# Optimization experiments

Hardware: AMD Instinct MI355X
Metric: run time of the kernel (lower is better)

## Reference

```python
import jax, jax.numpy as jnp
import numpy as np

E = 8          # num_experts
D = 768        # d_model
H = 3072       # d_hidden
TOP_K = 2


def setup_inputs() -> dict:
    key = jax.random.key(0)
    ks = jax.random.split(key, 8)
    s_in = 1.0 / np.sqrt(D)
    s_h = 1.0 / np.sqrt(H)
    return {
        "hidden_states": jax.random.normal(ks[0], (2, 2048, D), dtype=jnp.float32),
        "gate_w": jax.random.normal(ks[1], (E, D), dtype=jnp.float32) * s_in,
        "gate_b": jnp.zeros((E,), dtype=jnp.float32),
        "w1": jax.random.normal(ks[2], (E, H, D), dtype=jnp.float32) * s_in,  # FMoELinear: [E, out, in]
        "b1": jnp.zeros((E, H), dtype=jnp.float32),
        "w2": jax.random.normal(ks[3], (E, D, H), dtype=jnp.float32) * s_h,
        "b2": jnp.zeros((E, D), dtype=jnp.float32),
        "bias": jnp.zeros((D,), dtype=jnp.float32),
    }


def reference(hidden_states, gate_w, gate_b, w1, b1, w2, b2, bias):
    B, S, d = hidden_states.shape
    x = hidden_states.reshape(-1, d)                      # [T, D]
    T = x.shape[0]
    # NaiveGate: linear gate, top-k, softmax over the top-k logits
    logits = x @ gate_w.T + gate_b                        # [T, E]
    top_val, top_idx = jax.lax.top_k(logits, TOP_K)       # [T, K]
    scores = jax.nn.softmax(top_val, axis=-1)             # [T, K]
    # combine weights: [T, E], score mass scattered to chosen experts
    combine = jnp.zeros((T, E), dtype=x.dtype)
    combine = combine.at[jnp.arange(T)[:, None], top_idx].add(scores)
    # expert MLPs (dense over experts, masked combine keeps routing math exact)
    h = jnp.einsum('td,ehd->teh', x, w1) + b1             # [T, E, H]
    h = jax.nn.gelu(h, approximate=False)                 # torch F.gelu (exact erf)
    y = jnp.einsum('teh,edh->ted', h, w2) + b2            # [T, E, D]
    out = jnp.einsum('te,ted->td', combine, y)            # [T, D]
    return out.reshape(B, S, d), bias
```

## Files before the change

kernel.cpp:

```cpp
#include <hip/hip_runtime.h>
#include <hip/hip_bf16.h>

#define DD 768
#define HH 3072
#define NE 8
#define TOPK 2

#define BK 64
#define CAP 1536
#define NRBMAX (CAP/128)
#define NB1 (HH / 128)
#define NB2 (DD / 128)

typedef __attribute__((ext_vector_type(8))) short short8;
typedef __attribute__((ext_vector_type(4))) float f32x4;

static __device__ __forceinline__ unsigned short f2bf(float v) {
    __hip_bfloat16 b = __float2bfloat16(v);
    return *reinterpret_cast<unsigned short*>(&b);
}

static __device__ __forceinline__ float gelu_f(float v) {
    float s = v * 0.70710678118f;
    float a = fabsf(s);
    float t = __builtin_amdgcn_rcpf(1.f + 0.3275911f * a);
    float poly = t * (0.254829592f + t * (-0.284496736f + t * (1.421413741f +
                 t * (-1.453152027f + t * 1.061405429f))));
    float erfv = 1.f - poly * __expf(-s * s);
    erfv = copysignf(erfv, s);
    return 0.5f * v * (1.f + erfv);
}

__global__ __launch_bounds__(256) void convert_kernel(
    const float* __restrict__ w1, const float* __restrict__ w2,
    unsigned short* __restrict__ w1b, unsigned short* __restrict__ w2b,
    int* __restrict__ ctrl, int* __restrict__ qcur, size_t n)
{
    size_t tid = (size_t)blockIdx.x * blockDim.x + threadIdx.x;
    if (tid < 64) ctrl[tid] = 0;
    if (tid < 256) qcur[tid] = 0;
    size_t stride = (size_t)gridDim.x * blockDim.x;
    size_t quarter = n / 4;
    size_t tot = 2 * quarter;
    for (size_t j = tid; j < tot; j += stride) {
        const float* src; unsigned short* dst; size_t off;
        if (j < quarter) { src = w1; dst = w1b; off = j * 4; }
        else             { src = w2; dst = w2b; off = (j - quarter) * 4; }
        float4 v = *reinterpret_cast<const float4*>(&src[off]);
        ushort4 o;
        o.x = f2bf(v.x); o.y = f2bf(v.y); o.z = f2bf(v.z); o.w = f2bf(v.w);
        *reinterpret_cast<ushort4*>(&dst[off]) = o;
    }
}

__global__ __launch_bounds__(256) void route_kernel(
    const float* __restrict__ x, const float* __restrict__ gw, const float* __restrict__ gb,
    int* __restrict__ ctrl, int* __restrict__ pos_of, float* __restrict__ wpos,
    unsigned short* __restrict__ Xe, int T, int maxP)
{
    __shared__ int s_e[32], s_rank[32];
    __shared__ float s_w[32];
    __shared__ int lh[NE], lbase[NE];

    int tid = threadIdx.x;
    if (tid < NE) lh[tid] = 0;
    __syncthreads();

    int w = tid >> 6, lane = tid & 63;

#pragma unroll
    for (int j = 0; j < 4; ++j) {
        int t = blockIdx.x * 16 + w * 4 + j;
        if (t >= T) break;
        float acc[NE];
#pragma unroll
        for (int e = 0; e < NE; ++e) acc[e] = 0.f;
        const float4* xr = reinterpret_cast<const float4*>(x + (size_t)t * DD);
#pragma unroll
        for (int k = 0; k < 3; ++k) {
            float4 xv = xr[k * 64 + lane];
#pragma unroll
            for (int e = 0; e < NE; ++e) {
                float4 gv = *reinterpret_cast<const float4*>(&gw[e * DD + (k * 64 + lane) * 4]);
                acc[e] += xv.x * gv.x + xv.y * gv.y + xv.z * gv.z + xv.w * gv.w;
            }
        }
#pragma unroll
        for (int e = 0; e < NE; ++e) {
            float v = acc[e];
            for (int off = 32; off; off >>= 1) v += __shfl_xor(v, off, 64);
            acc[e] = v;
        }
        if (lane == 0) {
            float lg[NE];
#pragma unroll
            for (int e = 0; e < NE; ++e) lg[e] = acc[e] + gb[e];
            int i0 = 0;
#pragma unroll
            for (int e = 1; e < NE; ++e) if (lg[e] > lg[i0]) i0 = e;
            int i1 = -1;
#pragma unroll
            for (int e = 0; e < NE; ++e) {
                if (e == i0) continue;
                if (i1 < 0 || lg[e] > lg[i1]) i1 = e;
            }
            float m = lg[i0];
            float e0 = __expf(lg[i0] - m), e1 = __expf(lg[i1] - m);
            float s = e0 + e1;
            int slot = (w * 4 + j) * 2;
            s_e[slot]     = i0; s_w[slot]     = e0 / s; s_rank[slot]     = atomicAdd(&lh[i0], 1);
            s_e[slot + 1] = i1; s_w[slot + 1] = e1 / s; s_rank[slot + 1] = atomicAdd(&lh[i1], 1);
        }
    }
    __syncthreads();

    if (tid < NE) lbase[tid] = lh[tid] ? atomicAdd(&ctrl[8 + tid], lh[tid]) : 0;
    __syncthreads();

#pragma unroll
    for (int j = 0; j < 4; ++j) {
        int t = blockIdx.x * 16 + w * 4 + j;
        if (t >= T) break;
        const float4* xr = reinterpret_cast<const float4*>(x + (size_t)t * DD);
        ushort4 o[3];
#pragma unroll
        for (int k = 0; k < 3; ++k) {
            float4 v = xr[k * 64 + lane];
            o[k].x = f2bf(v.x); o[k].y = f2bf(v.y); o[k].z = f2bf(v.z); o[k].w = f2bf(v.w);
        }
#pragma unroll
        for (int s = 0; s < 2; ++s) {
            int slot = (w * 4 + j) * 2 + s;
            int e = s_e[slot];
            int p = e * CAP + lbase[e] + s_rank[slot];
            p = min(p, maxP - 1);
            if (lane == 0) { pos_of[2 * t + s] = p; wpos[p] = s_w[slot]; }
#pragma unroll
            for (int k = 0; k < 3; ++k)
                *reinterpret_cast<ushort4*>(&Xe[(size_t)p * DD + (k * 64 + lane) * 4]) = o[k];
        }
    }
}

__global__ void offsets_kernel(int* ctrl, int* wq1, int* wq2)
{
    if (threadIdx.x == 0 && blockIdx.x == 0) {
        int nrbs[NE];
        for (int e = 0; e < NE; ++e) {
            int cnt = ctrl[8 + e];
            int nrb = (cnt + 127) >> 7;
            nrbs[e] = nrb > NRBMAX ? NRBMAX : nrb;
        }
        int qc[8], qcum[8];
        for (int q = 0; q < 8; ++q) { qc[q] = 0; qcum[q] = 0; }
        for (int pair = 0; pair < NE * NB1; ++pair) {
            int e = pair / NB1;
            int q = pair & 7;
            int s = qc[q]++;
            qcum[q] += nrbs[e];
            wq1[(q * 24 + s) * 2 + 0] = pair;
            wq1[(q * 24 + s) * 2 + 1] = qcum[q];
        }
        for (int q = 0; q < 8; ++q) { qc[q] = 0; qcum[q] = 0; }
        for (int g = 0; g < NE * NB2; ++g) {
            int e = g / NB2;
            int q = g & 7;
            int s = qc[q]++;
            qcum[q] += nrbs[e];
            wq2[(q * 6 + s) * 2 + 0] = g;
            wq2[(q * 6 + s) * 2 + 1] = qcum[q];
        }
    }
}

static __device__ __forceinline__ void stage_tile(
    const unsigned short* __restrict__ g, int ld, unsigned short* __restrict__ lds)
{
    int tid = threadIdx.x;
#pragma unroll
    for (int r = 0; r < 4; ++r) {
        int j = (r << 8) + tid;
        int row = j >> 3;
        int kc = (j & 7) ^ (row & 7);
        __builtin_amdgcn_global_load_lds(
            (const __attribute__((address_space(1))) void*)(g + (size_t)row * ld + (kc << 3)),
            (__attribute__((address_space(3))) void*)(lds + (j << 3)),
            16, 0, 0);
    }
}

#define LDSF(base, row, kc) \
    reinterpret_cast<const short8*>(&(base)[((((row) << 3) + ((kc) ^ ((row) & 7))) << 3)])

static __device__ __forceinline__ void gemm_item(
    const unsigned short* __restrict__ Abase,
    const unsigned short* __restrict__ Bbase,
    int ld, int nt,
    unsigned short* __restrict__ As, unsigned short* __restrict__ Bs,
    f32x4 acc[4][4], int wr, int wc, int fr, int fq)
{
    const int BUF = 128 * 64;
    stage_tile(Abase, ld, As);
    stage_tile(Bbase, ld, Bs);
    for (int t = 0; t < nt; ++t) {
        int cur = t & 1;
        if (t + 1 < nt) {
            stage_tile(Abase + (size_t)(t + 1) * BK, ld, As + (cur ^ 1) * BUF);
            stage_tile(Bbase + (size_t)(t + 1) * BK, ld, Bs + (cur ^ 1) * BUF);
            asm volatile("s_waitcnt vmcnt(8)" ::: "memory");
        } else {
            asm volatile("s_waitcnt vmcnt(0)" ::: "memory");
        }
        __builtin_amdgcn_s_barrier();
        asm volatile("" ::: "memory");

        const unsigned short* A = As + cur * BUF;
        const unsigned short* B = Bs + cur * BUF;
        short8 a[2][4], b[2][4];
#pragma unroll
        for (int ks = 0; ks < 2; ++ks) {
            int kc = ks * 4 + fq;
#pragma unroll
            for (int m = 0; m < 4; ++m)
                a[ks][m] = *LDSF(A, wr + m * 16 + fr, kc);
#pragma unroll
            for (int n = 0; n < 4; ++n)
                b[ks][n] = *LDSF(B, wc + n * 16 + fr, kc);
        }
        __builtin_amdgcn_s_setprio(1);
#pragma unroll
        for (int ks = 0; ks < 2; ++ks)
#pragma unroll
            for (int m = 0; m < 4; ++m)
#pragma unroll
                for (int n = 0; n < 4; ++n)
                    acc[m][n] = __builtin_amdgcn_mfma_f32_16x16x32_bf16(
                        b[ks][n], a[ks][m], acc[m][n], 0, 0, 0);
        __builtin_amdgcn_s_setprio(0);
        asm volatile("s_waitcnt lgkmcnt(0)" ::: "memory");
        __builtin_amdgcn_s_barrier();
        asm volatile("" ::: "memory");
    }
}


__global__ __launch_bounds__(256, 2) void gemm1_kernel(
    const unsigned short* __restrict__ Xe, const unsigned short* __restrict__ W1b,
    const float* __restrict__ b1, unsigned short* __restrict__ H1,
    const int* __restrict__ wq1, int* __restrict__ qcur)
{
    __shared__ unsigned short As[2 * 128 * 64];
    __shared__ unsigned short Bs[2 * 128 * 64];
    __shared__ int sh_item;
    __shared__ int tpair[192], tcum[192];

    int tid = threadIdx.x;
    if (tid < 192) { tpair[tid] = wq1[2 * tid]; tcum[tid] = wq1[2 * tid + 1]; }
    __syncthreads();

    int lane = tid & 63, w = tid >> 6;
    int wr = (w >> 1) * 64, wc = (w & 1) * 64;
    int fr = lane & 15, fq = lane >> 4;
    int q0 = blockIdx.x & 7;

    for (int off = 0; off < 8; ++off) {
        int qq = (q0 + off) & 7;
        int qtot = tcum[qq * 24 + 23];
        for (;;) {
            if (tid == 0) sh_item = atomicAdd(&qcur[qq * 16], 1);
            __syncthreads();
            int j = sh_item;
            __syncthreads();
            if (j >= qtot) break;

            int s = 0;
            while (tcum[qq * 24 + s] <= j) ++s;
            int pair = tpair[qq * 24 + s];
            int start = s ? tcum[qq * 24 + s - 1] : 0;
            int rb = j - start;
            int e = pair / NB1, cb = pair - e * NB1;
            int rowbase = e * CAP + (rb << 7);
            int colbase = cb << 7;

            const unsigned short* Abase = Xe + (size_t)rowbase * DD;
            const unsigned short* Bbase = W1b + (size_t)e * HH * DD + (size_t)colbase * DD;

            f32x4 acc[4][4];
#pragma unroll
            for (int m = 0; m < 4; ++m)
#pragma unroll
                for (int n = 0; n < 4; ++n) acc[m][n] = (f32x4){0.f, 0.f, 0.f, 0.f};

            gemm_item(Abase, Bbase, DD, DD / BK, As, Bs, acc, wr, wc, fr, fq);

            float4 bb[4];
#pragma unroll
            for (int n = 0; n < 4; ++n)
                bb[n] = *reinterpret_cast<const float4*>(
                    &b1[e * HH + colbase + wc + n * 16 + fq * 4]);
#pragma unroll
            for (int m = 0; m < 4; ++m) {
                int tok = rowbase + wr + m * 16 + fr;
#pragma unroll
                for (int n = 0; n < 4; ++n) {
                    int ch = colbase + wc + n * 16 + fq * 4;
                    ushort4 o;
                    o.x = f2bf(gelu_f(acc[m][n][0] + bb[n].x));
                    o.y = f2bf(gelu_f(acc[m][n][1] + bb[n].y));
                    o.z = f2bf(gelu_f(acc[m][n][2] + bb[n].z));
                    o.w = f2bf(gelu_f(acc[m][n][3] + bb[n].w));
                    *reinterpret_cast<ushort4*>(&H1[(size_t)tok * HH + ch]) = o;
                }
            }
        }
    }
}

__global__ __launch_bounds__(256, 2) void gemm2_kernel(
    const unsigned short* __restrict__ H1, const unsigned short* __restrict__ W2b,
    const float* __restrict__ b2, const float* __restrict__ wpos,
    float* __restrict__ Yb, const int* __restrict__ wq2, int* __restrict__ qcur)
{
    __shared__ unsigned short As[2 * 128 * 64];
    __shared__ unsigned short Bs[2 * 128 * 64];
    __shared__ int sh_item;
    __shared__ int tpair[48], tcum[48];

    int tid = threadIdx.x;
    if (tid < 48) { tpair[tid] = wq2[2 * tid]; tcum[tid] = wq2[2 * tid + 1]; }
    __syncthreads();

    int lane = tid & 63, w = tid >> 6;
    int wr = (w >> 1) * 64, wc = (w & 1) * 64;
    int fr = lane & 15, fq = lane >> 4;
    int q0 = blockIdx.x & 7;

    for (int off = 0; off < 8; ++off) {
        int qq = (q0 + off) & 7;
        int qtot = tcum[qq * 6 + 5];
        for (;;) {
            if (tid == 0) sh_item = atomicAdd(&qcur[(8 + qq) * 16], 1);
            __syncthreads();
            int j = sh_item;
            __syncthreads();
            if (j >= qtot) break;

            int s = 0;
            while (tcum[qq * 6 + s] <= j) ++s;
            int g = tpair[qq * 6 + s];
            int start = s ? tcum[qq * 6 + s - 1] : 0;
            int rb = j - start;
            int e = g / NB2, cb = g - e * NB2;
            int rowbase = e * CAP + (rb << 7);
            int colbase = cb << 7;

            const unsigned short* Abase = H1 + (size_t)rowbase * HH;
            const unsigned short* Bbase = W2b + (size_t)e * DD * HH + (size_t)colbase * HH;

            f32x4 acc[4][4];
#pragma unroll
            for (int m = 0; m < 4; ++m)
#pragma unroll
                for (int n = 0; n < 4; ++n) acc[m][n] = (f32x4){0.f, 0.f, 0.f, 0.f};

            gemm_item(Abase, Bbase, HH, HH / BK, As, Bs, acc, wr, wc, fr, fq);

            float4 bb[4];
#pragma unroll
            for (int n = 0; n < 4; ++n)
                bb[n] = *reinterpret_cast<const float4*>(
                    &b2[e * DD + colbase + wc + n * 16 + fq * 4]);
#pragma unroll
            for (int m = 0; m < 4; ++m) {
                int tok = rowbase + wr + m * 16 + fr;
                float wp = wpos[tok];
#pragma unroll
                for (int n = 0; n < 4; ++n) {
                    int ch = colbase + wc + n * 16 + fq * 4;
                    float4 o;
                    o.x = wp * (acc[m][n][0] + bb[n].x);
                    o.y = wp * (acc[m][n][1] + bb[n].y);
                    o.z = wp * (acc[m][n][2] + bb[n].z);
                    o.w = wp * (acc[m][n][3] + bb[n].w);
                    *reinterpret_cast<float4*>(&Yb[(size_t)tok * DD + ch]) = o;
                }
            }
        }
    }
}

__global__ __launch_bounds__(256) void combine_kernel(
    const float* __restrict__ Yb, const int* __restrict__ pos_of,
    const float* __restrict__ bias, float* __restrict__ out, int T)
{
    int i = blockIdx.x * blockDim.x + threadIdx.x;
    int total = T * (DD / 4);
    if (i < total) {
        int t = i / (DD / 4);
        int c = (i % (DD / 4)) * 4;
        int p0 = pos_of[2 * t], p1 = pos_of[2 * t + 1];
        float4 v0 = *reinterpret_cast<const float4*>(&Yb[(size_t)p0 * DD + c]);
        float4 v1 = *reinterpret_cast<const float4*>(&Yb[(size_t)p1 * DD + c]);
        float4 o;
        o.x = v0.x + v1.x; o.y = v0.y + v1.y;
        o.z = v0.z + v1.z; o.w = v0.w + v1.w;
        *reinterpret_cast<float4*>(&out[(size_t)t * DD + c]) = o;
    } else if (i < total + DD / 4) {
        int c = (i - total) * 4;
        *reinterpret_cast<float4*>(&out[(size_t)T * DD + c]) =
            *reinterpret_cast<const float4*>(&bias[c]);
    }
}

extern "C" void kernel_launch(void* const* d_in, const int* in_sizes, int n_in,
                              void* d_out, int out_size, void* d_ws, size_t ws_size,
                              hipStream_t stream)
{
    const float* x    = (const float*)d_in[0];
    const float* gw   = (const float*)d_in[1];
    const float* gb   = (const float*)d_in[2];
    const float* w1   = (const float*)d_in[3];
    const float* b1   = (const float*)d_in[4];
    const float* w2   = (const float*)d_in[5];
    const float* b2   = (const float*)d_in[6];
    const float* bias = (const float*)d_in[7];
    float* out = (float*)d_out;

    int T = in_sizes[0] / DD;
    int nA = T * TOPK;
    int maxP = NE * CAP + 256;

    char* ws = (char*)d_ws;
    size_t off = 0;
    auto alloc = [&](size_t bytes) -> char* {
        char* p = ws + off;
        off += (bytes + 255) & ~(size_t)255;
        return p;
    };
    unsigned short* w1b = (unsigned short*)alloc((size_t)NE * HH * DD * 2);
    unsigned short* w2b = (unsigned short*)alloc((size_t)NE * DD * HH * 2);
    unsigned short* Xe  = (unsigned short*)alloc((size_t)maxP * DD * 2);
    unsigned short* H1  = (unsigned short*)alloc((size_t)maxP * HH * 2);
    float*  Yb          = (float*)alloc((size_t)maxP * DD * 4);
    int*    pos_of      = (int*)alloc((size_t)nA * 4);
    float*  wpos        = (float*)alloc((size_t)maxP * 4);
    int*    ctrl        = (int*)alloc(64 * 4);
    int*    wq1         = (int*)alloc(384 * 4);
    int*    wq2         = (int*)alloc(96 * 4);
    int*    qcur        = (int*)alloc(256 * 4);

    size_t nW = (size_t)NE * HH * DD;

    hipLaunchKernelGGL(convert_kernel, dim3(4096), dim3(256), 0, stream,
                       w1, w2, w1b, w2b, ctrl, qcur, nW);
    hipLaunchKernelGGL(route_kernel, dim3((T + 15) / 16), dim3(256), 0, stream,
                       x, gw, gb, ctrl, pos_of, wpos, Xe, T, maxP);
    hipLaunchKernelGGL(offsets_kernel, dim3(1), dim3(64), 0, stream, ctrl, wq1, wq2);
    hipLaunchKernelGGL(gemm1_kernel, dim3(512), dim3(256), 0, stream,
                       Xe, w1b, b1, H1, wq1, qcur);
    hipLaunchKernelGGL(gemm2_kernel, dim3(512), dim3(256), 0, stream,
                       H1, w2b, b2, wpos, Yb, wq2, qcur);
    hipLaunchKernelGGL(combine_kernel, dim3((T * (DD / 4) + DD / 4 + 255) / 256, 1, 1), dim3(256), 0, stream,
                       Yb, pos_of, bias, out, T);
}
```

Before: 240.2 us.

## Fuse weight conversion into routing and gemm1 tails to overlap with compute

Removes the standalone fp32-to-bf16 conversion kernel. The w1 conversion now runs inside the routing kernel on a grid of at least 2048 blocks, and the w2 conversion runs as work-stealing tail chunks at the end of gemm1, claimed through an atomic counter. Control counters are zeroed with memsets instead. The aim is to hide conversion bandwidth behind routing and the gemm1 tail and to save a launch, at the cost of extra gemm1 work and possible contention with its memory traffic.

```diff
diff --git a/kernel.cpp b/kernel.cpp
--- a/kernel.cpp
+++ b/kernel.cpp
@@ -31,115 +31,108 @@
     return 0.5f * v * (1.f + erfv);
 }
 
-__global__ __launch_bounds__(256) void convert_kernel(
-    const float* __restrict__ w1, const float* __restrict__ w2,
-    unsigned short* __restrict__ w1b, unsigned short* __restrict__ w2b,
-    int* __restrict__ ctrl, int* __restrict__ qcur, size_t n)
-{
-    size_t tid = (size_t)blockIdx.x * blockDim.x + threadIdx.x;
-    if (tid < 64) ctrl[tid] = 0;
-    if (tid < 256) qcur[tid] = 0;
-    size_t stride = (size_t)gridDim.x * blockDim.x;
-    size_t quarter = n / 4;
-    size_t tot = 2 * quarter;
-    for (size_t j = tid; j < tot; j += stride) {
-        const float* src; unsigned short* dst; size_t off;
-        if (j < quarter) { src = w1; dst = w1b; off = j * 4; }
-        else             { src = w2; dst = w2b; off = (j - quarter) * 4; }
-        float4 v = *reinterpret_cast<const float4*>(&src[off]);
-        ushort4 o;
-        o.x = f2bf(v.x); o.y = f2bf(v.y); o.z = f2bf(v.z); o.w = f2bf(v.w);
-        *reinterpret_cast<ushort4*>(&dst[off]) = o;
-    }
-}
-
-__global__ __launch_bounds__(256) void route_kernel(
+static __device__ __forceinline__ void cvt4(const float* __restrict__ src,
+                                            unsigned short* __restrict__ dst, size_t j4)
+{
+    float4 v = *reinterpret_cast<const float4*>(&src[j4 * 4]);
+    ushort4 o;
+    o.x = f2bf(v.x); o.y = f2bf(v.y); o.z = f2bf(v.z); o.w = f2bf(v.w);
+    *reinterpret_cast<ushort4*>(&dst[j4 * 4]) = o;
+}
+
+__global__ __launch_bounds__(256) void routecvt_kernel(
     const float* __restrict__ x, const float* __restrict__ gw, const float* __restrict__ gb,
     int* __restrict__ ctrl, int* __restrict__ pos_of, float* __restrict__ wpos,
-    unsigned short* __restrict__ Xe, int T, int maxP)
+    unsigned short* __restrict__ Xe, int T, int maxP,
+    const float* __restrict__ w1, unsigned short* __restrict__ w1b, size_t n1_4)
 {
     __shared__ int s_e[32], s_rank[32];
     __shared__ float s_w[32];
     __shared__ int lh[NE], lbase[NE];
 
     int tid = threadIdx.x;
-    if (tid < NE) lh[tid] = 0;
-    __syncthreads();
-
     int w = tid >> 6, lane = tid & 63;
 
-#pragma unroll
-    for (int j = 0; j < 4; ++j) {
-        int t = blockIdx.x * 16 + w * 4 + j;
-        if (t >= T) break;
-        float acc[NE];
-#pragma unroll
-        for (int e = 0; e < NE; ++e) acc[e] = 0.f;
-        const float4* xr = reinterpret_cast<const float4*>(x + (size_t)t * DD);
-#pragma unroll
-        for (int k = 0; k < 3; ++k) {
-            float4 xv = xr[k * 64 + lane];
+    if ((int)blockIdx.x * 16 < T) {
+        if (tid < NE) lh[tid] = 0;
+        __syncthreads();
+
+#pragma unroll
+        for (int j = 0; j < 4; ++j) {
+            int t = blockIdx.x * 16 + w * 4 + j;
+            if (t >= T) break;
+            float acc[NE];
+#pragma unroll
+            for (int e = 0; e < NE; ++e) acc[e] = 0.f;
+            const float4* xr = reinterpret_cast<const float4*>(x + (size_t)t * DD);
+#pragma unroll
+            for (int k = 0; k < 3; ++k) {
+                float4 xv = xr[k * 64 + lane];
+#pragma unroll
+                for (int e = 0; e < NE; ++e) {
+                    float4 gv = *reinterpret_cast<const float4*>(&gw[e * DD + (k * 64 + lane) * 4]);
+                    acc[e] += xv.x * gv.x + xv.y * gv.y + xv.z * gv.z + xv.w * gv.w;
+                }
+            }
 #pragma unroll
             for (int e = 0; e < NE; ++e) {
-                float4 gv = *reinterpret_cast<const float4*>(&gw[e * DD + (k * 64 + lane) * 4]);
-                acc[e] += xv.x * gv.x + xv.y * gv.y + xv.z * gv.z + xv.w * gv.w;
-            }
-        }
-#pragma unroll
-        for (int e = 0; e < NE; ++e) {
-            float v = acc[e];
-            for (int off = 32; off; off >>= 1) v += __shfl_xor(v, off, 64);
-            acc[e] = v;
-        }
-        if (lane == 0) {
-            float lg[NE];
-#pragma unroll
-            for (int e = 0; e < NE; ++e) lg[e] = acc[e] + gb[e];
-            int i0 = 0;
-#pragma unroll
-            for (int e = 1; e < NE; ++e) if (lg[e] > lg[i0]) i0 = e;
-            int i1 = -1;
-#pragma unroll
-            for (int e = 0; e < NE; ++e) {
-                if (e == i0) continue;
-                if (i1 < 0 || lg[e] > lg[i1]) i1 = e;
-            }
-            float m = lg[i0];
-            float e0 = __expf(lg[i0] - m), e1 = __expf(lg[i1] - m);
-            float s = e0 + e1;
-            int slot = (w * 4 + j) * 2;
-            s_e[slot]     = i0; s_w[slot]     = e0 / s; s_rank[slot]     = atomicAdd(&lh[i0], 1);
-            s_e[slot + 1] = i1; s_w[slot + 1] = e1 / s; s_rank[slot + 1] = atomicAdd(&lh[i1], 1);
-        }
-    }
-    __syncthreads();
-
-    if (tid < NE) lbase[tid] = lh[tid] ? atomicAdd(&ctrl[8 + tid], lh[tid]) : 0;
-    __syncthreads();
-
-#pragma unroll
-    for (int j = 0; j < 4; ++j) {
-        int t = blockIdx.x * 16 + w * 4 + j;
-        if (t >= T) break;
-        const float4* xr = reinterpret_cast<const float4*>(x + (size_t)t * DD);
-        ushort4 o[3];
-#pragma unroll
-        for (int k = 0; k < 3; ++k) {
-            float4 v = xr[k * 64 + lane];
-            o[k].x = f2bf(v.x); o[k].y = f2bf(v.y); o[k].z = f2bf(v.z); o[k].w = f2bf(v.w);
-        }
-#pragma unroll
-        for (int s = 0; s < 2; ++s) {
-            int slot = (w * 4 + j) * 2 + s;
-            int e = s_e[slot];
-            int p = e * CAP + lbase[e] + s_rank[slot];
-            p = min(p, maxP - 1);
-            if (lane == 0) { pos_of[2 * t + s] = p; wpos[p] = s_w[slot]; }
-#pragma unroll
-            for (int k = 0; k < 3; ++k)
-                *reinterpret_cast<ushort4*>(&Xe[(size_t)p * DD + (k * 64 + lane) * 4]) = o[k];
-        }
-    }
+                float v = acc[e];
+                for (int off = 32; off; off >>= 1) v += __shfl_xor(v, off, 64);
+                acc[e] = v;
+            }
+            if (lane == 0) {
+                float lg[NE];
+#pragma unroll
+                for (int e = 0; e < NE; ++e) lg[e] = acc[e] + gb[e];
+                int i0 = 0;
+#pragma unroll
+                for (int e = 1; e < NE; ++e) if (lg[e] > lg[i0]) i0 = e;
+                int i1 = -1;
+#pragma unroll
+                for (int e = 0; e < NE; ++e) {
+                    if (e == i0) continue;
+                    if (i1 < 0 || lg[e] > lg[i1]) i1 = e;
+                }
+                float m = lg[i0];
+                float e0 = __expf(lg[i0] - m), e1 = __expf(lg[i1] - m);
+                float s = e0 + e1;
+                int slot = (w * 4 + j) * 2;
+                s_e[slot]     = i0; s_w[slot]     = e0 / s; s_rank[slot]     = atomicAdd(&lh[i0], 1);
+                s_e[slot + 1] = i1; s_w[slot + 1] = e1 / s; s_rank[slot + 1] = atomicAdd(&lh[i1], 1);
+            }
+        }
+        __syncthreads();
+
+        if (tid < NE) lbase[tid] = lh[tid] ? atomicAdd(&ctrl[8 + tid], lh[tid]) : 0;
+        __syncthreads();
+
+#pragma unroll
+        for (int j = 0; j < 4; ++j) {
+            int t = blockIdx.x * 16 + w * 4 + j;
+            if (t >= T) break;
+            const float4* xr = reinterpret_cast<const float4*>(x + (size_t)t * DD);
+            ushort4 o[3];
+#pragma unroll
+            for (int k = 0; k < 3; ++k) {
+                float4 v = xr[k * 64 + lane];
+                o[k].x = f2bf(v.x); o[k].y = f2bf(v.y); o[k].z = f2bf(v.z); o[k].w = f2bf(v.w);
+            }
+#pragma unroll
+            for (int s = 0; s < 2; ++s) {
+                int slot = (w * 4 + j) * 2 + s;
+                int e = s_e[slot];
+                int p = e * CAP + lbase[e] + s_rank[slot];
+                p = min(p, maxP - 1);
+                if (lane == 0) { pos_of[2 * t + s] = p; wpos[p] = s_w[slot]; }
+#pragma unroll
+                for (int k = 0; k < 3; ++k)
+                    *reinterpret_cast<ushort4*>(&Xe[(size_t)p * DD + (k * 64 + lane) * 4]) = o[k];
+            }
+        }
+    }
+
+    for (size_t j = (size_t)blockIdx.x * 256 + tid; j < n1_4; j += (size_t)gridDim.x * 256)
+        cvt4(w1, w1b, j);
 }
 
 __global__ void offsets_kernel(int* ctrl, int* wq1, int* wq2)
@@ -247,7 +240,8 @@
 __global__ __launch_bounds__(256, 2) void gemm1_kernel(
     const unsigned short* __restrict__ Xe, const unsigned short* __restrict__ W1b,
     const float* __restrict__ b1, unsigned short* __restrict__ H1,
-    const int* __restrict__ wq1, int* __restrict__ qcur)
+    const int* __restrict__ wq1, int* __restrict__ qcur,
+    const float* __restrict__ w2, unsigned short* __restrict__ w2b, size_t n2_4)
 {
     __shared__ unsigned short As[2 * 128 * 64];
     __shared__ unsigned short Bs[2 * 128 * 64];
@@ -312,6 +306,20 @@
                     *reinterpret_cast<ushort4*>(&H1[(size_t)tok * HH + ch]) = o;
                 }
             }
+        }
+    }
+
+    for (;;) {
+        if (tid == 0) sh_item = atomicAdd(&qcur[255], 1);
+        __syncthreads();
+        int c = sh_item;
+        __syncthreads();
+        size_t base = (size_t)c * 4096;
+        if (base >= n2_4) break;
+#pragma unroll
+        for (int k = 0; k < 16; ++k) {
+            size_t j = base + k * 256 + tid;
+            if (j < n2_4) cvt4(w2, w2b, j);
         }
     }
 }
@@ -450,14 +458,18 @@
     int*    qcur        = (int*)alloc(256 * 4);
 
     size_t nW = (size_t)NE * HH * DD;
-
-    hipLaunchKernelGGL(convert_kernel, dim3(4096), dim3(256), 0, stream,
-                       w1, w2, w1b, w2b, ctrl, qcur, nW);
-    hipLaunchKernelGGL(route_kernel, dim3((T + 15) / 16), dim3(256), 0, stream,
-                       x, gw, gb, ctrl, pos_of, wpos, Xe, T, maxP);
+    size_t nW4 = nW / 4;
+
+    hipMemsetAsync(ctrl, 0, 64 * 4, stream);
+    hipMemsetAsync(qcur, 0, 256 * 4, stream);
+
+    int routeBlocks = (T + 15) / 16;
+    int rcGrid = routeBlocks > 2048 ? routeBlocks : 2048;
+    hipLaunchKernelGGL(routecvt_kernel, dim3(rcGrid), dim3(256), 0, stream,
+                       x, gw, gb, ctrl, pos_of, wpos, Xe, T, maxP, w1, w1b, nW4);
     hipLaunchKernelGGL(offsets_kernel, dim3(1), dim3(64), 0, stream, ctrl, wq1, wq2);
     hipLaunchKernelGGL(gemm1_kernel, dim3(512), dim3(256), 0, stream,
-                       Xe, w1b, b1, H1, wq1, qcur);
+                       Xe, w1b, b1, H1, wq1, qcur, w2, w2b, nW4);
     hipLaunchKernelGGL(gemm2_kernel, dim3(512), dim3(256), 0, stream,
                        H1, w2b, b2, wpos, Yb, wq2, qcur);
     hipLaunchKernelGGL(combine_kernel, dim3((T * (DD / 4) + DD / 4 + 255) / 256, 1, 1), dim3(256), 0, stream,
```

Result: no change. 239.5 us (-0.3%).
